# Kernel tuning notes

Measured on AMD Instinct MI355X. Metric: run time of the kernel, lower is better.

## Reference

```python
import jax, jax.numpy as jnp
import numpy as np
import math

D = 1024      # d_model
DC = 256      # d_cache
DL = DC // 4  # d_layer
K = 64        # num_slots
NL = 8        # num_layers
N = NL * K    # cache slots (L*K)
P = 16        # num_patterns
H = 16        # num_heads
B, S = 8, 1024
F = 4 * D

def _linear(x, w, b):
    return jnp.matmul(x, w.T) + b

def _ln(x, g, b):
    m = jnp.mean(x, -1, keepdims=True)
    v = jnp.mean((x - m) ** 2, -1, keepdims=True)
    return (x - m) * jax.lax.rsqrt(v + 1e-5) * g + b

def _mha(q, k, v, wqkv, bqkv, wo, bo, nh):
    # torch nn.MultiheadAttention (batch_first, eval/no-dropout)
    d = q.shape[-1]; dh = d // nh
    wq, wk, wv = jnp.split(wqkv, 3, axis=0)
    bq, bk, bv = jnp.split(bqkv, 3, axis=0)
    qh = _linear(q, wq, bq).reshape(q.shape[0], q.shape[1], nh, dh)
    kh = _linear(k, wk, bk).reshape(k.shape[0], k.shape[1], nh, dh)
    vh = _linear(v, wv, bv).reshape(v.shape[0], v.shape[1], nh, dh)
    s = jnp.einsum('bqhd,bkhd->bhqk', qh, kh) * (1.0 / math.sqrt(dh))
    a = jax.nn.softmax(s, axis=-1)
    o = jnp.einsum('bhqk,bkhd->bqhd', a, vh).reshape(q.shape[0], q.shape[1], d)
    return _linear(o, wo, bo)

def _forward(x, cache, slot_embeddings, layer_ids, gumbel_u, layer_embed,
             attn_wqkv, attn_bqkv, attn_wo, attn_bo,
             pat_wqkv, pat_bqkv, pat_wo, pat_bo, pattern_queries,
             ffn_w1, ffn_b1, ffn_w2, ffn_b2,
             n1_g, n1_b, n2_g, n2_b,
             gate_w, gate_b, sel_w, sel_b, sq_w, sq_b, sk_w, sk_b, an_w, an_b,
             dec_w, dec_b, cq_w, cq_b, ck_w, ck_b, cv_w, cv_b, fg_w, fg_b):
    b, s, d = x.shape
    # --- read_cache: cross-attention from tokens to [B,N,DC] cache slots ---
    cid = jnp.concatenate([cache, jnp.broadcast_to(layer_ids[None], (b,) + layer_ids.shape)], axis=-1)  # [B,N,DC+DL]
    q = _linear(x, cq_w, cq_b)                    # [B,S,DC]
    kk = _linear(cid, ck_w, ck_b)                 # [B,N,DC]
    vv = _linear(cid, cv_w, cv_b)                 # [B,N,DC]
    sc = jnp.einsum('bsd,bnd->bsn', q, kk) * (1.0 / math.sqrt(DC))
    attn = jax.nn.softmax(sc, axis=-1)
    ctx = jnp.einsum('bsn,bnd->bsd', attn, vv)    # [B,S,DC]
    ctx = jnp.concatenate([ctx, jnp.broadcast_to(layer_embed, (b, s, layer_embed.shape[-1]))], axis=-1)
    context = _linear(ctx, dec_w, dec_b)          # [B,S,D]
    # --- gated fusion ---
    gate = jax.nn.sigmoid(_linear(jnp.concatenate([x, context], axis=-1), fg_w, fg_b))
    xf = gate * x + (1.0 - gate) * context
    # --- self-attn + FFN transformer block ---
    xf = _ln(xf + _mha(xf, xf, xf, attn_wqkv, attn_bqkv, attn_wo, attn_bo, H), n1_g, n1_b)
    ffn = _linear(jax.nn.gelu(_linear(xf, ffn_w1, ffn_b1), approximate=False), ffn_w2, ffn_b2)
    y = _ln(xf + ffn, n2_g, n2_b)
    # --- pattern pooling ---
    queries = jnp.broadcast_to(pattern_queries[None], (b,) + pattern_queries.shape)
    patterns = _mha(queries, y, y, pat_wqkv, pat_bqkv, pat_wo, pat_bo, H)   # [B,P,D]
    # --- selection head (hybrid routing + gumbel-softmax, soft mode) ---
    scores = jax.nn.sigmoid(_linear(patterns, gate_w, gate_b))[..., 0]      # [B,P]
    learned = _linear(patterns, sel_w, sel_b)                               # [B,P,K]
    content = jnp.einsum('bpd,kd->bpk', _linear(patterns, sq_w, sq_b),
                         _linear(slot_embeddings, sk_w, sk_b)) * (1.0 / math.sqrt(DC))
    alpha = jax.nn.sigmoid(_linear(patterns, an_w, an_b))                   # [B,P,1]
    logits = alpha * learned + (1.0 - alpha) * content
    g = -jnp.log(-jnp.log(gumbel_u + 1e-8) + 1e-8)
    slot_probs = jax.nn.softmax(logits + g, axis=-1)  # temperature = 1.0, hard=False
    soft_probs = jax.nn.softmax(logits, axis=-1)
    return y, patterns, scores, slot_probs, soft_probs, alpha[..., 0]

def setup_inputs() -> dict:
    key = jax.random.key(0)
    ks = iter(jax.random.split(key, 64))
    def rn(shape, scale=1.0):
        return scale * jax.random.normal(next(ks), shape, dtype=jnp.float32)
    inp = {
        'x': rn((B, S, D)),
        'cache': rn((B, N, DC)),
        'slot_embeddings': rn((K, DC), 0.02),
        'layer_ids': rn((N, DL), 0.02),
        'gumbel_u': jax.random.uniform(next(ks), (B, P, K), dtype=jnp.float32, minval=1e-4, maxval=1.0),
        'layer_embed': rn((1, 1, DL), 0.02),
        'attn_wqkv': rn((3 * D, D), 0.02), 'attn_bqkv': jnp.zeros((3 * D,)),
        'attn_wo': rn((D, D), 0.02), 'attn_bo': jnp.zeros((D,)),
        'pat_wqkv': rn((3 * D, D), 0.02), 'pat_bqkv': jnp.zeros((3 * D,)),
        'pat_wo': rn((D, D), 0.02), 'pat_bo': jnp.zeros((D,)),
        'pattern_queries': rn((P, D), 0.02),
        'ffn_w1': rn((F, D), 0.02), 'ffn_b1': jnp.zeros((F,)),
        'ffn_w2': rn((D, F), 0.02), 'ffn_b2': jnp.zeros((D,)),
        'n1_g': jnp.ones((D,)), 'n1_b': jnp.zeros((D,)),
        'n2_g': jnp.ones((D,)), 'n2_b': jnp.zeros((D,)),
        'gate_w': rn((1, D), 0.02), 'gate_b': jnp.zeros((1,)),
        'sel_w': rn((K, D), 0.02), 'sel_b': jnp.zeros((K,)),
        'sq_w': rn((DC, D), 0.02), 'sq_b': jnp.zeros((DC,)),
        'sk_w': rn((DC, DC), 0.02), 'sk_b': jnp.zeros((DC,)),
        'an_w': rn((1, D), 0.02), 'an_b': jnp.zeros((1,)),
        'dec_w': rn((D, DC + DL), 0.02), 'dec_b': jnp.zeros((D,)),
        'cq_w': rn((DC, D), 0.02), 'cq_b': jnp.zeros((DC,)),
        'ck_w': rn((DC, DC + DL), 0.02), 'ck_b': jnp.zeros((DC,)),
        'cv_w': rn((DC, DC + DL), 0.02), 'cv_b': jnp.zeros((DC,)),
        'fg_w': rn((D, 2 * D), 0.02), 'fg_b': jnp.zeros((D,)),
    }
    return inp

def reference(x, cache, slot_embeddings, layer_ids, gumbel_u, layer_embed,
              attn_wqkv, attn_bqkv, attn_wo, attn_bo,
              pat_wqkv, pat_bqkv, pat_wo, pat_bo, pattern_queries,
              ffn_w1, ffn_b1, ffn_w2, ffn_b2,
              n1_g, n1_b, n2_g, n2_b,
              gate_w, gate_b, sel_w, sel_b, sq_w, sq_b, sk_w, sk_b, an_w, an_b,
              dec_w, dec_b, cq_w, cq_b, ck_w, ck_b, cv_w, cv_b, fg_w, fg_b):
    return _forward(x, cache, slot_embeddings, layer_ids, gumbel_u, layer_embed,
                    attn_wqkv, attn_bqkv, attn_wo, attn_bo,
                    pat_wqkv, pat_bqkv, pat_wo, pat_bo, pattern_queries,
                    ffn_w1, ffn_b1, ffn_w2, ffn_b2,
                    n1_g, n1_b, n2_g, n2_b,
                    gate_w, gate_b, sel_w, sel_b, sq_w, sq_b, sk_w, sk_b, an_w, an_b,
                    dec_w, dec_b, cq_w, cq_b, ck_w, ck_b, cv_w, cv_b, fg_w, fg_b)
```

## Files before the change

kernel.cpp:

```cpp
#include <hip/hip_runtime.h>
#include <math.h>

typedef unsigned short u16;
typedef unsigned int u32;
typedef __bf16 bfx8 __attribute__((ext_vector_type(8)));
typedef float fx4 __attribute__((ext_vector_type(4)));

__device__ __forceinline__ float b2f(u16 v) { return __uint_as_float(((u32)v) << 16); }
__device__ __forceinline__ u16 f2b(float f) {
    u32 u = __float_as_uint(f);
    u32 lsb = (u >> 16) & 1u;
    u += 0x7fffu + lsb;
    return (u16)(u >> 16);
}
__device__ __forceinline__ float4 unpack4(u32 a, u32 b) {
    float4 r;
    r.x = __uint_as_float(a << 16);
    r.y = __uint_as_float(a & 0xffff0000u);
    r.z = __uint_as_float(b << 16);
    r.w = __uint_as_float(b & 0xffff0000u);
    return r;
}
__device__ __forceinline__ float sigmoid_(float x) { return 1.f / (1.f + __expf(-x)); }
__device__ __forceinline__ float gelu_(float x) { return 0.5f * x * (1.f + erff(x * 0.7071067811865475f)); }

__device__ __forceinline__ float ldx(const void* p, long i, int f) {
    return f ? ((const float*)p)[i] : b2f(((const u16*)p)[i]);
}
__device__ __forceinline__ void stx(void* p, long i, float v, int f) {
    if (f) ((float*)p)[i] = v;
    else ((u16*)p)[i] = f2b(v);
}
__device__ __forceinline__ void stage8(u16* dst, const void* src, long idx, int f, bool ok) {
    uint4 r;
    if (!ok) {
        r = make_uint4(0u, 0u, 0u, 0u);
    } else if (f) {
        const float* p = (const float*)src + idx;
        float4 a = *(const float4*)p;
        float4 b = *(const float4*)(p + 4);
        r = make_uint4((u32)f2b(a.x) | ((u32)f2b(a.y) << 16),
                       (u32)f2b(a.z) | ((u32)f2b(a.w) << 16),
                       (u32)f2b(b.x) | ((u32)f2b(b.y) << 16),
                       (u32)f2b(b.z) | ((u32)f2b(b.w) << 16));
    } else {
        r = *(const uint4*)((const u16*)src + idx);
    }
    *(uint4*)dst = r;
}

__device__ __forceinline__ void glds16(const u16* g, u16* l) {
    __builtin_amdgcn_global_load_lds(
        (const __attribute__((address_space(1))) u32*)g,
        (__attribute__((address_space(3))) u32*)l, 16, 0, 0);
}

__global__ void detect_dtype(const u16* __restrict__ n1g, int* __restrict__ flag) {
    *flag = (n1g[0] == 0) ? 1 : 0;
}

__global__ __launch_bounds__(256) void conv_weights(
    const void* awqkv, const void* awo, const void* fw1, const void* fw2,
    const void* pwqkv, const void* fgw, const void* decw, const void* cqw,
    const void* ckw, const void* x, u16* __restrict__ dst, const int* __restrict__ flagp)
{
    const int f = *flagp;
    long c = ((long)blockIdx.x * 256 + threadIdx.x) * 8;
    if (c >= 25837568L) return;
    const void* src; long off;
    if      (c < 3145728L)  { src = awqkv; off = c; }
    else if (c < 4194304L)  { src = awo;   off = c - 3145728L; }
    else if (c < 8388608L)  { src = fw1;   off = c - 4194304L; }
    else if (c < 12582912L) { src = fw2;   off = c - 8388608L; }
    else if (c < 14680064L) { src = pwqkv; off = c - 12582912L + 1048576L; }
    else if (c < 16777216L) { src = fgw;   off = c - 14680064L; }
    else if (c < 17104896L) { src = decw;  off = c - 16777216L; }
    else if (c < 17367040L) { src = cqw;   off = c - 17104896L; }
    else if (c < 17448960L) { src = ckw;   off = c - 17367040L; }
    else                    { src = x;     off = c - 17448960L; }
    uint4 r;
    if (f) {
        const float* p = (const float*)src + off;
        float4 a = *(const float4*)p;
        float4 b = *(const float4*)(p + 4);
        r = make_uint4((u32)f2b(a.x) | ((u32)f2b(a.y) << 16),
                       (u32)f2b(a.z) | ((u32)f2b(a.w) << 16),
                       (u32)f2b(b.x) | ((u32)f2b(b.y) << 16),
                       (u32)f2b(b.z) | ((u32)f2b(b.w) << 16));
    } else {
        r = *(const uint4*)((const u16*)src + off);
    }
    *(uint4*)(dst + c) = r;
}

template <int ACT, int ACC>
__global__ __launch_bounds__(256) void gemm_big(
    const u16* __restrict__ A, const u16* __restrict__ B, const void* __restrict__ bias,
    u16* __restrict__ C, int M, int N, int K, int lda, int ldb, int ldc, float scale,
    long aS, long bS, long cS, long biasBase, const int* __restrict__ flagp)
{
    const int f = *flagp;
    const long z = blockIdx.z;
    const u16* Ab = A + z * aS;
    const u16* Bb = B + z * bS;
    u16* Cb = C + z * cS;

    __shared__ u16 As[8192];
    __shared__ u16 Bs[8192];

    const int tid = threadIdx.x;
    const int w = tid >> 6;
    const int lane = tid & 63;
    const int l15 = lane & 15;
    const int quad = lane >> 4;
    const int wr = w >> 1, wc = w & 1;

    const int m0 = blockIdx.y * 128;
    const int n0 = blockIdx.x * 128;

    const int srow = lane >> 3;
    const int scol = ((lane & 7) ^ srow) << 3;

    fx4 acc[4][4];
#pragma unroll
    for (int mi = 0; mi < 4; ++mi)
#pragma unroll
        for (int ni = 0; ni < 4; ++ni) {
            fx4 zz = {0.f, 0.f, 0.f, 0.f};
            acc[mi][ni] = zz;
        }

    for (int k0 = 0; k0 < K; k0 += 64) {
        __syncthreads();
#pragma unroll
        for (int j = 0; j < 4; ++j) {
            const int rg = (j * 4 + w) * 8 + srow;
            glds16(Ab + (long)(m0 + rg) * lda + k0 + scol, &As[(j * 4 + w) * 512]);
            glds16(Bb + (long)(n0 + rg) * ldb + k0 + scol, &Bs[(j * 4 + w) * 512]);
        }
        __syncthreads();
#pragma unroll
        for (int kk = 0; kk < 2; ++kk) {
            bfx8 af[4], bf[4];
#pragma unroll
            for (int i = 0; i < 4; ++i) {
                const int ar = wr * 64 + i * 16 + l15;
                af[i] = *(const bfx8*)((const char*)As + ar * 128 +
                                       ((kk * 64 + quad * 16) ^ ((ar & 7) << 4)));
                const int br = wc * 64 + i * 16 + l15;
                bf[i] = *(const bfx8*)((const char*)Bs + br * 128 +
                                       ((kk * 64 + quad * 16) ^ ((br & 7) << 4)));
            }
#pragma unroll
            for (int mi = 0; mi < 4; ++mi)
#pragma unroll
                for (int ni = 0; ni < 4; ++ni)
                    acc[mi][ni] = __builtin_amdgcn_mfma_f32_16x16x32_bf16(af[mi], bf[ni], acc[mi][ni], 0, 0, 0);
        }
    }

#pragma unroll
    for (int ni = 0; ni < 4; ++ni) {
        const int col = n0 + wc * 64 + ni * 16 + l15;
        const float bv = bias ? ldx(bias, biasBase + col, f) : 0.f;
#pragma unroll
        for (int mi = 0; mi < 4; ++mi) {
            const int row = m0 + wr * 64 + mi * 16 + quad * 4;
#pragma unroll
            for (int r = 0; r < 4; ++r) {
                float v = acc[mi][ni][r] * scale + bv;
                if (ACT) v = gelu_(v);
                long idx = (long)(row + r) * ldc + col;
                if (ACC) v += b2f(Cb[idx]);
                Cb[idx] = f2b(v);
            }
        }
    }
}

template <int OUTF32, int ACT, int TRANS, int ACC>
__global__ __launch_bounds__(256) void gemm_nt(
    const void* __restrict__ A, const void* __restrict__ B, const void* __restrict__ bias,
    void* __restrict__ Cv, int M, int N, int K, int lda, int ldb, int ldc, float scale,
    long aBase, long aDiv, long aOut, long aIn,
    long bBase, long bDiv, long bOut, long bIn,
    long cDiv, long cOut, long cIn,
    long biasBase, int aIsIn, int bIsIn, int biasIsIn, const int* __restrict__ flagp)
{
    const int dfl = *flagp;
    const int af = aIsIn ? dfl : 0;
    const int bfF = bIsIn ? dfl : 0;
    const int sf = biasIsIn ? dfl : 0;

    long bi = blockIdx.z;
    const long aOff = aBase + (bi / aDiv) * aOut + (bi % aDiv) * aIn;
    const long bOff = bBase + (bi / bDiv) * bOut + (bi % bDiv) * bIn;
    const long cOff = (bi / cDiv) * cOut + (bi % cDiv) * cIn;

    __shared__ u16 As[64][40];
    __shared__ u16 Bs[64][40];

    const int tid = threadIdx.x;
    const int w = tid >> 6;
    const int lane = tid & 63;
    const int m0 = blockIdx.y * 64;
    const int n0 = blockIdx.x * 64;

    const int lr = tid >> 2;
    const int lk = (tid & 3) * 8;

    fx4 acc[4];
#pragma unroll
    for (int c = 0; c < 4; ++c)
#pragma unroll
        for (int r = 0; r < 4; ++r) acc[c][r] = 0.f;

    const int arow = m0 + lr;
    const int brow = n0 + lr;
    const bool aok = arow < M;
    const bool bok = brow < N;

    const int row16 = lane & 15;
    const int quad = lane >> 4;

    for (int k0 = 0; k0 < K; k0 += 32) {
        __syncthreads();
        stage8(&As[lr][lk], A, aOff + (long)arow * lda + k0 + lk, af, aok);
        stage8(&Bs[lr][lk], B, bOff + (long)brow * ldb + k0 + lk, bfF, bok);
        __syncthreads();
        bfx8 afr = *(const bfx8*)&As[w * 16 + row16][quad * 8];
#pragma unroll
        for (int c = 0; c < 4; ++c) {
            bfx8 bfr = *(const bfx8*)&Bs[c * 16 + row16][quad * 8];
            acc[c] = __builtin_amdgcn_mfma_f32_16x16x32_bf16(afr, bfr, acc[c], 0, 0, 0);
        }
    }

#pragma unroll
    for (int c = 0; c < 4; ++c) {
        int col = n0 + c * 16 + row16;
        float bvv = bias ? ldx(bias, biasBase + col, sf) : 0.f;
#pragma unroll
        for (int r = 0; r < 4; ++r) {
            int row = m0 + w * 16 + quad * 4 + r;
            if (row < M) {
                float v = acc[c][r] * scale + bvv;
                if (ACT == 1) v = gelu_(v);
                long idx = TRANS ? ((long)col * ldc + row) : ((long)row * ldc + col);
                if (OUTF32) {
                    ((float*)Cv)[cOff + idx] = v;
                } else {
                    if (ACC) v += b2f(((u16*)Cv)[cOff + idx]);
                    ((u16*)Cv)[cOff + idx] = f2b(v);
                }
            }
        }
    }
}

__global__ __launch_bounds__(256) void attn_self(const u16* __restrict__ QKV, u16* __restrict__ O,
                                                 int ldo, long bStride)
{
    const int h = blockIdx.y;
    const long zoff = (long)blockIdx.z * bStride;
    const u16* Qb = QKV + zoff + h * 64;
    const u16* Kb = Qb + 1024;
    const u16* Vb = Qb + 2048;
    u16* Ob = O + zoff + h * 64;

    const int tid = threadIdx.x;
    const int w = tid >> 6;
    const int lane = tid & 63;
    const int l15 = lane & 15;
    const int quad = lane >> 4;
    const int q0 = blockIdx.x * 64;

    __shared__ u16 Ks[64][72];
    __shared__ u16 Vt[64][72];
    __shared__ u16 Ps[4][16][72];

    bfx8 aq[2];
    {
        const u16* qrow = Qb + (long)(q0 + w * 16 + l15) * 3072 + quad * 8;
        aq[0] = *(const bfx8*)(qrow);
        aq[1] = *(const bfx8*)(qrow + 32);
    }

    fx4 acc[4];
#pragma unroll
    for (int c = 0; c < 4; ++c) {
        fx4 z = {0.f, 0.f, 0.f, 0.f};
        acc[c] = z;
    }
    float m[4], l[4];
#pragma unroll
    for (int r = 0; r < 4; ++r) { m[r] = -__builtin_inff(); l[r] = 0.f; }

    const int sr = tid >> 2;
    const int sc = (tid & 3) * 16;
    const int vr = lane;
    const int vc = w * 16;

    for (int kt = 0; kt < 16; ++kt) {
        __syncthreads();
        {
            const uint4* kp = (const uint4*)(Kb + (long)(kt * 64 + sr) * 3072 + sc);
            *(uint4*)&Ks[sr][sc] = kp[0];
            *(uint4*)&Ks[sr][sc + 8] = kp[1];
        }
        {
            const u16* vp = Vb + (long)(kt * 64 + vr) * 3072 + vc;
            uint4 a = *(const uint4*)vp;
            uint4 b = *(const uint4*)(vp + 8);
            u16 tmp[16];
            *(uint4*)&tmp[0] = a;
            *(uint4*)&tmp[8] = b;
#pragma unroll
            for (int j = 0; j < 16; ++j) Vt[vc + j][vr] = tmp[j];
        }
        __syncthreads();

        fx4 s[4];
#pragma unroll
        for (int c = 0; c < 4; ++c) {
            bfx8 b0 = *(const bfx8*)&Ks[c * 16 + l15][quad * 8];
            bfx8 b1 = *(const bfx8*)&Ks[c * 16 + l15][32 + quad * 8];
            fx4 t = {0.f, 0.f, 0.f, 0.f};
            t = __builtin_amdgcn_mfma_f32_16x16x32_bf16(aq[0], b0, t, 0, 0, 0);
            t = __builtin_amdgcn_mfma_f32_16x16x32_bf16(aq[1], b1, t, 0, 0, 0);
            s[c] = t;
        }
#pragma unroll
        for (int c = 0; c < 4; ++c)
#pragma unroll
            for (int r = 0; r < 4; ++r) s[c][r] *= 0.125f;

#pragma unroll
        for (int r = 0; r < 4; ++r) {
            float tm = fmaxf(fmaxf(s[0][r], s[1][r]), fmaxf(s[2][r], s[3][r]));
#pragma unroll
            for (int off = 1; off < 16; off <<= 1) tm = fmaxf(tm, __shfl_xor(tm, off));
            if (tm > m[r]) {
                float al = __expf(m[r] - tm);
                l[r] *= al;
#pragma unroll
                for (int c = 0; c < 4; ++c) acc[c][r] *= al;
                m[r] = tm;
            }
            float rs = 0.f;
#pragma unroll
            for (int c = 0; c < 4; ++c) {
                float p = __expf(s[c][r] - m[r]);
                s[c][r] = p;
                rs += p;
            }
#pragma unroll
            for (int off = 1; off < 16; off <<= 1) rs += __shfl_xor(rs, off);
            l[r] += rs;
        }

#pragma unroll
        for (int c = 0; c < 4; ++c)
#pragma unroll
            for (int r = 0; r < 4; ++r)
                Ps[w][quad * 4 + r][c * 16 + l15] = f2b(s[c][r]);

#pragma unroll
        for (int ks = 0; ks < 2; ++ks) {
            bfx8 ap = *(const bfx8*)&Ps[w][l15][ks * 32 + quad * 8];
#pragma unroll
            for (int c = 0; c < 4; ++c) {
                bfx8 bv = *(const bfx8*)&Vt[c * 16 + l15][ks * 32 + quad * 8];
                acc[c] = __builtin_amdgcn_mfma_f32_16x16x32_bf16(ap, bv, acc[c], 0, 0, 0);
            }
        }
    }

#pragma unroll
    for (int r = 0; r < 4; ++r) {
        float inv = 1.f / l[r];
        u16* op = Ob + (long)(q0 + w * 16 + quad * 4 + r) * ldo;
#pragma unroll
        for (int c = 0; c < 4; ++c)
            op[c * 16 + l15] = f2b(acc[c][r] * inv);
    }
}

__global__ __launch_bounds__(256) void softmax_inplace(u16* __restrict__ d, int W)
{
    long row = blockIdx.x;
    u16* r = d + row * W;
    int t = threadIdx.x;
    int n = W >> 8;
    float v[4];
    float mx = -1e30f;
    for (int i = 0; i < n; ++i) { v[i] = b2f(r[t + 256 * i]); mx = fmaxf(mx, v[i]); }
    __shared__ float red[256];
    red[t] = mx; __syncthreads();
    for (int s = 128; s > 0; s >>= 1) { if (t < s) red[t] = fmaxf(red[t], red[t + s]); __syncthreads(); }
    mx = red[0]; __syncthreads();
    float sum = 0.f;
    for (int i = 0; i < n; ++i) { v[i] = __expf(v[i] - mx); sum += v[i]; }
    red[t] = sum; __syncthreads();
    for (int s = 128; s > 0; s >>= 1) { if (t < s) red[t] += red[t + s]; __syncthreads(); }
    float inv = 1.f / red[0];
    for (int i = 0; i < n; ++i) r[t + 256 * i] = f2b(v[i] * inv);
}

__global__ __launch_bounds__(256) void add_ln(const u16* __restrict__ a, const u16* __restrict__ rres,
                                              const void* __restrict__ g, const void* __restrict__ be,
                                              u16* __restrict__ o1, void* __restrict__ o2, long o2off,
                                              const int* __restrict__ flagp)
{
    const int f = *flagp;
    long row = blockIdx.x;
    int t = threadIdx.x;
    const u16* ar = a + row * 1024;
    const u16* rr = rres + row * 1024;
    float v[4];
#pragma unroll
    for (int i = 0; i < 4; ++i) { int j = t + 256 * i; v[i] = b2f(ar[j]) + b2f(rr[j]); }
    __shared__ float red[256];
    float s = v[0] + v[1] + v[2] + v[3];
    red[t] = s; __syncthreads();
    for (int k = 128; k > 0; k >>= 1) { if (t < k) red[t] += red[t + k]; __syncthreads(); }
    float mean = red[0] * (1.f / 1024.f);
    __syncthreads();
    float sq = 0.f;
#pragma unroll
    for (int i = 0; i < 4; ++i) { float d = v[i] - mean; sq += d * d; }
    red[t] = sq; __syncthreads();
    for (int k = 128; k > 0; k >>= 1) { if (t < k) red[t] += red[t + k]; __syncthreads(); }
    float rs = rsqrtf(red[0] * (1.f / 1024.f) + 1e-5f);
#pragma unroll
    for (int i = 0; i < 4; ++i) {
        int j = t + 256 * i;
        float y = (v[i] - mean) * rs * ldx(g, j, f) + ldx(be, j, f);
        o1[row * 1024 + j] = f2b(y);
        if (o2) stx(o2, o2off + row * 1024 + j, y, f);
    }
}

__global__ __launch_bounds__(256) void build_cid(const void* __restrict__ cache, const void* __restrict__ lids,
                                                 u16* __restrict__ cid, const int* __restrict__ flagp)
{
    const int f = *flagp;
    long i = (long)blockIdx.x * 256 + threadIdx.x;
    if (i >= 4096L * 320) return;
    long row = i / 320, c = i % 320;
    float v = (c < 256) ? ldx(cache, row * 256 + c, f) : ldx(lids, (row & 511) * 64 + (c - 256), f);
    cid[i] = f2b(v);
}

__global__ __launch_bounds__(256) void fill_ctx_le(const void* __restrict__ le, u16* __restrict__ ctxcat,
                                                   const int* __restrict__ flagp)
{
    const int f = *flagp;
    long i = (long)blockIdx.x * 256 + threadIdx.x;
    if (i >= 8192L * 64) return;
    long row = i >> 6, j = i & 63;
    ctxcat[row * 320 + 256 + j] = f2b(ldx(le, j, f));
}

__global__ __launch_bounds__(256) void fusion(const void* __restrict__ x, const u16* __restrict__ ctx,
                                              u16* __restrict__ gl_xf, const int* __restrict__ flagp)
{
    const int f = *flagp;
    long i = (long)blockIdx.x * 256 + threadIdx.x;
    float gv = sigmoid_(b2f(gl_xf[i]));
    float xv = ldx(x, i, f);
    float cv = b2f(ctx[i]);
    gl_xf[i] = f2b(gv * xv + (1.f - gv) * cv);
}

__global__ __launch_bounds__(256) void cast_pat(const float* __restrict__ pf, u16* __restrict__ pb,
                                                void* __restrict__ pout, long poff,
                                                const int* __restrict__ flagp)
{
    const int f = *flagp;
    long i = (long)blockIdx.x * 256 + threadIdx.x;
    if (i >= 131072L) return;
    float v = pf[i];
    pb[i] = f2b(v);
    stx(pout, poff + i, v, f);
}

__global__ __launch_bounds__(64) void pat_pv(const u16* __restrict__ patp, const u16* __restrict__ kv,
                                             u16* __restrict__ opat, long pStride, long kvStride, long oStride)
{
    int qi = blockIdx.x, h = blockIdx.y, z = blockIdx.z, t = threadIdx.x;
    const u16* prow = patp + (long)z * pStride + ((long)(h * 16 + qi)) * 1024;
    const u16* v = kv + (long)z * kvStride + 1024 + h * 64 + t;
    float o = 0.f;
#pragma unroll 4
    for (int key = 0; key < 1024; ++key) o += b2f(prow[key]) * b2f(v[(long)key * 2048]);
    opat[(long)z * oStride + (long)qi * 1024 + h * 64 + t] = f2b(o);
}

__global__ __launch_bounds__(64) void final_head(const u16* __restrict__ patb, const float* __restrict__ learned,
                                                 const float* __restrict__ content, const void* __restrict__ gum,
                                                 const void* __restrict__ gw, const void* __restrict__ gb,
                                                 const void* __restrict__ anw, const void* __restrict__ anb,
                                                 void* __restrict__ outp, long oSC, long oSLOT, long oSOFT, long oAL,
                                                 const int* __restrict__ flagp)
{
    const int f = *flagp;
    int row = blockIdx.x;
    int t = threadIdx.x;
    float pa = 0.f, ps = 0.f;
    for (int j = t; j < 1024; j += 64) {
        float p = b2f(patb[(long)row * 1024 + j]);
        pa += p * ldx(anw, j, f);
        ps += p * ldx(gw, j, f);
    }
#pragma unroll
    for (int off = 32; off > 0; off >>= 1) { pa += __shfl_xor(pa, off); ps += __shfl_xor(ps, off); }
    float alpha = sigmoid_(pa + ldx(anb, 0, f));
    float score = sigmoid_(ps + ldx(gb, 0, f));
    float logit = alpha * learned[row * 64 + t] + (1.f - alpha) * content[row * 64 + t];
    float u = ldx(gum, row * 64 + t, f);
    float inner = -logf(u + 1e-8f) + 1e-8f;
    inner = fmaxf(inner, 1e-20f);
    float gg = -logf(inner);
    float l1 = logit + gg, l2 = logit;
    float m1 = l1, m2 = l2;
#pragma unroll
    for (int off = 32; off > 0; off >>= 1) { m1 = fmaxf(m1, __shfl_xor(m1, off)); m2 = fmaxf(m2, __shfl_xor(m2, off)); }
    float e1 = __expf(l1 - m1), e2 = __expf(l2 - m2);
    float s1 = e1, s2 = e2;
#pragma unroll
    for (int off = 32; off > 0; off >>= 1) { s1 += __shfl_xor(s1, off); s2 += __shfl_xor(s2, off); }
    stx(outp, oSLOT + row * 64 + t, e1 / s1, f);
    stx(outp, oSOFT + row * 64 + t, e2 / s2, f);
    if (t == 0) { stx(outp, oSC + row, score, f); stx(outp, oAL + row, alpha, f); }
}

static void launch_gemm(hipStream_t st, int outf32, int act, int trans, int acc,
                        const void* A, const void* B, const void* bias, void* C,
                        int M, int N, int K, int lda, int ldb, int ldc, float scale, int batch,
                        long aBase, long aD, long aO, long aI,
                        long bBase, long bD, long bO, long bI,
                        long cD, long cO, long cI,
                        long biasBase, int aIsIn, int bIsIn, int biasIsIn, const int* flagp)
{
    dim3 g(N / 64, (M + 63) / 64, batch);
#define PASS A, B, bias, C, M, N, K, lda, ldb, ldc, scale, aBase, aD, aO, aI, bBase, bD, bO, bI, \
             cD, cO, cI, biasBase, aIsIn, bIsIn, biasIsIn, flagp
    if (outf32)      gemm_nt<1, 0, 0, 0><<<g, 256, 0, st>>>(PASS);
    else if (act)    gemm_nt<0, 1, 0, 0><<<g, 256, 0, st>>>(PASS);
    else if (trans)  gemm_nt<0, 0, 1, 0><<<g, 256, 0, st>>>(PASS);
    else if (acc)    gemm_nt<0, 0, 0, 1><<<g, 256, 0, st>>>(PASS);
    else             gemm_nt<0, 0, 0, 0><<<g, 256, 0, st>>>(PASS);
#undef PASS
}

static void launch_big(hipStream_t st, int act, int acc,
                       const u16* A, const u16* B, const void* bias, u16* C,
                       int M, int N, int K, int lda, int ldb, int ldc, float scale, int batch,
                       long aS, long bS, long cS, long biasBase, const int* flagp)
{
    dim3 g(N / 128, M / 128, batch);
#define PASSB A, B, bias, C, M, N, K, lda, ldb, ldc, scale, aS, bS, cS, biasBase, flagp
    if (act)      gemm_big<1, 0><<<g, 256, 0, st>>>(PASSB);
    else if (acc) gemm_big<0, 1><<<g, 256, 0, st>>>(PASSB);
    else          gemm_big<0, 0><<<g, 256, 0, st>>>(PASSB);
#undef PASSB
}

#define WS_CID     0L
#define WS_QB      2621440L
#define WS_KKB     6815744L
#define WS_VVT     8912896L
#define WS_SC      11010048L
#define WS_CTXCAT  0L
#define WS_CONTEXT 16777216L
#define WS_XF      0L

#define CS_QKVB    33554432L
#define CS_PROJ    16777216L
#define CS_FFN1C   16777216L
#define CS_FFN2C   33554432L
#define CS_KVPATB  16777216L
#define CS_QPAT    20971520L
#define CS_PATSC   21004288L
#define CS_OPAT    21528576L
#define CS_PATF32  21790720L
#define CS_PATB    22315008L
#define CS_LEARN   22577152L
#define CS_SQP     22609920L
#define CS_SKE     22675456L
#define CS_CONT    22708224L
#define CS_FLAG    39845888L
#define CS_NEED    39845892L

#define FP_QKV     33554432L
#define FP_PROJ    16777216L
#define FP_FFN1    33554432L
#define FP_FFN2    16777216L
#define FP_KVPAT   33554432L
#define FP_PATSC   16777216L
#define FP_QPAT    100663296L
#define FP_OPAT    100696064L
#define FP_PATF32  100958208L
#define FP_PATB    101482496L
#define FP_LEARN   101744640L
#define FP_SQP     101777408L
#define FP_SKE     101842944L
#define FP_CONT    101875712L
#define FP_FLAG    101908480L
#define FP_NEED    101908484L

#define FP2_WB     102760448L
#define WB_AWQKV   0L
#define WB_AWO     3145728L
#define WB_FW1     4194304L
#define WB_FW2     8388608L
#define WB_PWKV    12582912L
#define WB_FGW     14680064L
#define WB_DECW    16777216L
#define WB_CQW     17104896L
#define WB_CKW     17367040L
#define WB_X       17448960L
#define WB_TOTAL   25837568L
#define FP2_NEED   (FP2_WB + WB_TOTAL * 2)

#define OUT_Y      0L
#define OUT_PAT    8388608L
#define OUT_SCORES 8519680L
#define OUT_SLOT   8519808L
#define OUT_SOFT   8528000L
#define OUT_ALPHA  8536192L

extern "C" void kernel_launch(void* const* d_in, const int* in_sizes, int n_in,
                              void* d_out, int out_size, void* d_ws, size_t ws_size,
                              hipStream_t stream)
{
    const void* x     = d_in[0];
    const void* cache = d_in[1];
    const void* slote = d_in[2];
    const void* lids  = d_in[3];
    const void* gum   = d_in[4];
    const void* le    = d_in[5];
    const void* awqkv = d_in[6];
    const void* abqkv = d_in[7];
    const void* awo   = d_in[8];
    const void* abo   = d_in[9];
    const void* pwqkv = d_in[10];
    const void* pbqkv = d_in[11];
    const void* pwo   = d_in[12];
    const void* pbo   = d_in[13];
    const void* pq    = d_in[14];
    const void* fw1   = d_in[15];
    const void* fb1   = d_in[16];
    const void* fw2   = d_in[17];
    const void* fb2   = d_in[18];
    const void* n1g   = d_in[19];
    const void* n1b   = d_in[20];
    const void* n2g   = d_in[21];
    const void* n2b   = d_in[22];
    const void* gw    = d_in[23];
    const void* gb    = d_in[24];
    const void* selw  = d_in[25];
    const void* selb  = d_in[26];
    const void* sqw   = d_in[27];
    const void* sqb   = d_in[28];
    const void* skw   = d_in[29];
    const void* skb   = d_in[30];
    const void* anw   = d_in[31];
    const void* anb   = d_in[32];
    const void* decw  = d_in[33];
    const void* decb  = d_in[34];
    const void* cqw   = d_in[35];
    const void* cqb   = d_in[36];
    const void* ckw   = d_in[37];
    const void* ckb   = d_in[38];
    const void* cvw   = d_in[39];
    const void* cvb   = d_in[40];
    const void* fgw   = d_in[41];
    const void* fgb   = d_in[42];

    char* ws = (char*)d_ws;
    auto W  = [&](long off) { return (u16*)(ws + off); };
    auto Wf = [&](long off) { return (float*)(ws + off); };

    const bool fast = ws_size >= (size_t)FP_NEED;
    const bool fast2 = ws_size >= (size_t)FP2_NEED;
    int* flg = (int*)(ws + (fast ? FP_FLAG : CS_FLAG));
    u16* WB = (u16*)(ws + FP2_WB);
    const long oQPAT   = fast ? FP_QPAT   : CS_QPAT;
    const long oOPAT   = fast ? FP_OPAT   : CS_OPAT;
    const long oPATF32 = fast ? FP_PATF32 : CS_PATF32;
    const long oPATB   = fast ? FP_PATB   : CS_PATB;
    const long oLEARN  = fast ? FP_LEARN  : CS_LEARN;
    const long oSQP    = fast ? FP_SQP    : CS_SQP;
    const long oSKE    = fast ? FP_SKE    : CS_SKE;
    const long oCONT   = fast ? FP_CONT   : CS_CONT;

    detect_dtype<<<1, 1, 0, stream>>>((const u16*)n1g, flg);
    if (fast2)
        conv_weights<<<12616, 256, 0, stream>>>(awqkv, awo, fw1, fw2, pwqkv, fgw, decw, cqw, ckw, x, WB, flg);
    build_cid<<<dim3((4096 * 320 + 255) / 256), 256, 0, stream>>>(cache, lids, W(WS_CID), flg);
    if (fast2)
        launch_big(stream, 0, 0, WB + WB_X, WB + WB_CQW, cqb, W(WS_QB), 8192, 256, 1024,
                   1024, 1024, 256, 1.f, 1, 0, 0, 0, 0, flg);
    else
        launch_gemm(stream, 0, 0, 0, 0, x, cqw, cqb, W(WS_QB), 8192, 256, 1024, 1024, 1024, 256, 1.f, 1,
                    0, 1, 0, 0, 0, 1, 0, 0, 1, 0, 0, 0, 1, 1, 1, flg);
    if (fast2)
        launch_big(stream, 0, 0, W(WS_CID), WB + WB_CKW, ckb, W(WS_KKB), 4096, 256, 320,
                   320, 320, 256, 1.f, 1, 0, 0, 0, 0, flg);
    else
        launch_gemm(stream, 0, 0, 0, 0, W(WS_CID), ckw, ckb, W(WS_KKB), 4096, 256, 320, 320, 320, 256, 1.f, 1,
                    0, 1, 0, 0, 0, 1, 0, 0, 1, 0, 0, 0, 0, 1, 1, flg);
    launch_gemm(stream, 0, 0, 1, 0, W(WS_CID), cvw, cvb, W(WS_VVT), 512, 256, 320, 320, 320, 512, 1.f, 8,
                0, 1, 163840, 0, 0, 1, 0, 0, 1, 131072, 0, 0, 0, 1, 1, flg);
    if (fast2)
        launch_big(stream, 0, 0, W(WS_QB), W(WS_KKB), nullptr, W(WS_SC), 1024, 512, 256,
                   256, 256, 512, 0.0625f, 8, 262144, 131072, 524288, 0, flg);
    else
        launch_gemm(stream, 0, 0, 0, 0, W(WS_QB), W(WS_KKB), nullptr, W(WS_SC), 1024, 512, 256, 256, 256, 512,
                    0.0625f, 8, 0, 1, 262144, 0, 0, 1, 131072, 0, 1, 524288, 0, 0, 0, 0, 0, flg);
    softmax_inplace<<<8192, 256, 0, stream>>>(W(WS_SC), 512);
    if (fast2)
        launch_big(stream, 0, 0, W(WS_SC), W(WS_VVT), nullptr, W(WS_CTXCAT), 1024, 256, 512,
                   512, 512, 320, 1.f, 8, 524288, 131072, 327680, 0, flg);
    else
        launch_gemm(stream, 0, 0, 0, 0, W(WS_SC), W(WS_VVT), nullptr, W(WS_CTXCAT), 1024, 256, 512, 512, 512, 320,
                    1.f, 8, 0, 1, 524288, 0, 0, 1, 131072, 0, 1, 327680, 0, 0, 0, 0, 0, flg);
    fill_ctx_le<<<dim3((8192 * 64 + 255) / 256), 256, 0, stream>>>(le, W(WS_CTXCAT), flg);
    if (fast2)
        launch_big(stream, 0, 0, W(WS_CTXCAT), WB + WB_DECW, decb, W(WS_CONTEXT), 8192, 1024, 320,
                   320, 320, 1024, 1.f, 1, 0, 0, 0, 0, flg);
    else
        launch_gemm(stream, 0, 0, 0, 0, W(WS_CTXCAT), decw, decb, W(WS_CONTEXT), 8192, 1024, 320, 320, 320, 1024,
                    1.f, 1, 0, 1, 0, 0, 0, 1, 0, 0, 1, 0, 0, 0, 0, 1, 1, flg);
    if (fast2)
        launch_big(stream, 0, 0, WB + WB_X, WB + WB_FGW, fgb, W(WS_XF), 8192, 1024, 1024,
                   1024, 2048, 1024, 1.f, 1, 0, 0, 0, 0, flg);
    else
        launch_gemm(stream, 0, 0, 0, 0, x, fgw, fgb, W(WS_XF), 8192, 1024, 1024, 1024, 2048, 1024, 1.f, 1,
                    0, 1, 0, 0, 0, 1, 0, 0, 1, 0, 0, 0, 1, 1, 1, flg);
    if (fast2)
        launch_big(stream, 0, 1, W(WS_CONTEXT), WB + WB_FGW + 1024, nullptr, W(WS_XF), 8192, 1024, 1024,
                   1024, 2048, 1024, 1.f, 1, 0, 0, 0, 0, flg);
    else
        launch_gemm(stream, 0, 0, 0, 1, W(WS_CONTEXT), fgw, nullptr, W(WS_XF), 8192, 1024, 1024, 1024, 2048, 1024,
                    1.f, 1, 0, 1, 0, 0, 1024, 1, 0, 0, 1, 0, 0, 0, 0, 1, 0, flg);
    fusion<<<32768, 256, 0, stream>>>(x, W(WS_CONTEXT), W(WS_XF), flg);

    if (fast) {
        if (fast2)
            launch_big(stream, 0, 0, W(WS_XF), WB + WB_AWQKV, abqkv, W(FP_QKV), 8192, 3072, 1024,
                       1024, 1024, 3072, 1.f, 1, 0, 0, 0, 0, flg);
        else
            launch_gemm(stream, 0, 0, 0, 0, W(WS_XF), awqkv, abqkv, W(FP_QKV), 8192, 3072, 1024,
                        1024, 1024, 3072, 1.f, 1, 0, 1, 0, 0, 0, 1, 0, 0, 1, 0, 0, 0, 0, 1, 1, flg);
        attn_self<<<dim3(16, 16, 8), 256, 0, stream>>>(W(FP_QKV), W(FP_QKV), 3072, 3145728L);
        if (fast2)
            launch_big(stream, 0, 0, W(FP_QKV), WB + WB_AWO, abo, W(FP_PROJ), 8192, 1024, 1024,
                       3072, 1024, 1024, 1.f, 1, 0, 0, 0, 0, flg);
        else
            launch_gemm(stream, 0, 0, 0, 0, W(FP_QKV), awo, abo, W(FP_PROJ), 8192, 1024, 1024,
                        3072, 1024, 1024, 1.f, 1, 0, 1, 0, 0, 0, 1, 0, 0, 1, 0, 0, 0, 0, 1, 1, flg);
        add_ln<<<8192, 256, 0, stream>>>(W(WS_XF), W(FP_PROJ), n1g, n1b, W(WS_XF), nullptr, 0, flg);
        if (fast2)
            launch_big(stream, 1, 0, W(WS_XF), WB + WB_FW1, fb1, W(FP_FFN1), 8192, 4096, 1024,
                       1024, 1024, 4096, 1.f, 1, 0, 0, 0, 0, flg);
        else
            launch_gemm(stream, 0, 1, 0, 0, W(WS_XF), fw1, fb1, W(FP_FFN1), 8192, 4096, 1024,
                        1024, 1024, 4096, 1.f, 1, 0, 1, 0, 0, 0, 1, 0, 0, 1, 0, 0, 0, 0, 1, 1, flg);
        if (fast2)
            launch_big(stream, 0, 0, W(FP_FFN1), WB + WB_FW2, fb2, W(FP_FFN2), 8192, 1024, 4096,
                       4096, 4096, 1024, 1.f, 1, 0, 0, 0, 0, flg);
        else
            launch_gemm(stream, 0, 0, 0, 0, W(FP_FFN1), fw2, fb2, W(FP_FFN2), 8192, 1024, 4096,
                        4096, 4096, 1024, 1.f, 1, 0, 1, 0, 0, 0, 1, 0, 0, 1, 0, 0, 0, 0, 1, 1, flg);
        add_ln<<<8192, 256, 0, stream>>>(W(WS_XF), W(FP_FFN2), n2g, n2b, W(WS_XF), d_out, OUT_Y, flg);
        launch_gemm(stream, 0, 0, 0, 0, pq, pwqkv, pbqkv, W(oQPAT), 16, 1024, 1024, 1024, 1024, 1024, 1.f, 1,
                    0, 1, 0, 0, 0, 1, 0, 0, 1, 0, 0, 0, 1, 1, 1, flg);
        if (fast2)
            launch_big(stream, 0, 0, W(WS_XF), WB + WB_PWKV, pbqkv, W(FP_KVPAT), 8192, 2048, 1024,
                       1024, 1024, 2048, 1.f, 1, 0, 0, 0, 1024, flg);
        else
            launch_gemm(stream, 0, 0, 0, 0, W(WS_XF), pwqkv, pbqkv, W(FP_KVPAT), 8192, 2048, 1024,
                        1024, 1024, 2048, 1.f, 1, 0, 1, 0, 0, 1048576, 1, 0, 0, 1, 0, 0, 1024, 0, 1, 1, flg);
        launch_gemm(stream, 0, 0, 0, 0, W(oQPAT), W(FP_KVPAT), nullptr, W(FP_PATSC), 16, 1024, 64,
                    1024, 2048, 1024, 0.125f, 128,
                    0, 16, 0, 64, 0, 16, 2097152, 64, 1, 16384, 0, 0, 0, 0, 0, flg);
        softmax_inplace<<<2048, 256, 0, stream>>>(W(FP_PATSC), 1024);
        pat_pv<<<dim3(16, 16, 8), 64, 0, stream>>>(W(FP_PATSC), W(FP_KVPAT), W(oOPAT),
                                                   262144L, 2097152L, 16384L);
    } else {
        for (int b = 0; b < 8; ++b) {
            launch_gemm(stream, 0, 0, 0, 0, W(WS_XF) + (long)b * 1048576, awqkv, abqkv, W(CS_QKVB),
                        1024, 3072, 1024, 1024, 1024, 3072, 1.f, 1,
                        0, 1, 0, 0, 0, 1, 0, 0, 1, 0, 0, 0, 0, 1, 1, flg);
            attn_self<<<dim3(16, 16, 1), 256, 0, stream>>>(W(CS_QKVB), W(CS_QKVB), 3072, 0L);
            launch_gemm(stream, 0, 0, 0, 0, W(CS_QKVB), awo, abo, W(CS_PROJ) + (long)b * 1048576,
                        1024, 1024, 1024, 3072, 1024, 1024, 1.f, 1,
                        0, 1, 0, 0, 0, 1, 0, 0, 1, 0, 0, 0, 0, 1, 1, flg);
        }
        add_ln<<<8192, 256, 0, stream>>>(W(WS_XF), W(CS_PROJ), n1g, n1b, W(WS_XF), nullptr, 0, flg);
        for (int c = 0; c < 4; ++c) {
            u16* xf2c = W(WS_XF) + (long)c * 2048 * 1024;
            launch_gemm(stream, 0, 1, 0, 0, xf2c, fw1, fb1, W(CS_FFN1C), 2048, 4096, 1024, 1024, 1024, 4096,
                        1.f, 1, 0, 1, 0, 0, 0, 1, 0, 0, 1, 0, 0, 0, 0, 1, 1, flg);
            launch_gemm(stream, 0, 0, 0, 0, W(CS_FFN1C), fw2, fb2, W(CS_FFN2C), 2048, 1024, 4096,
                        4096, 4096, 1024, 1.f, 1, 0, 1, 0, 0, 0, 1, 0, 0, 1, 0, 0, 0, 0, 1, 1, flg);
            add_ln<<<2048, 256, 0, stream>>>(xf2c, W(CS_FFN2C), n2g, n2b, xf2c, d_out,
                                             OUT_Y + (long)c * 2048 * 1024, flg);
        }
        launch_gemm(stream, 0, 0, 0, 0, pq, pwqkv, pbqkv, W(oQPAT), 16, 1024, 1024, 1024, 1024, 1024, 1.f, 1,
                    0, 1, 0, 0, 0, 1, 0, 0, 1, 0, 0, 0, 1, 1, 1, flg);
        for (int b = 0; b < 8; ++b) {
            const u16* yb = W(WS_XF) + (long)b * 1048576;
            launch_gemm(stream, 0, 0, 0, 0, yb, pwqkv, pbqkv, W(CS_KVPATB), 1024, 2048, 1024,
                        1024, 1024, 2048, 1.f, 1, 0, 1, 0, 0, 1048576, 1, 0, 0, 1, 0, 0, 1024, 0, 1, 1, flg);
            launch_gemm(stream, 0, 0, 0, 0, W(oQPAT), W(CS_KVPATB), nullptr, W(CS_PATSC), 16, 1024, 64,
                        1024, 2048, 1024, 0.125f, 16,
                        0, 16, 0, 64, 0, 16, 0, 64, 1, 16384, 0, 0, 0, 0, 0, flg);
            softmax_inplace<<<256, 256, 0, stream>>>(W(CS_PATSC), 1024);
            pat_pv<<<dim3(16, 16, 1), 64, 0, stream>>>(W(CS_PATSC), W(CS_KVPATB),
                                                       W(oOPAT) + (long)b * 16384, 0L, 0L, 0L);
        }
    }

    launch_gemm(stream, 1, 0, 0, 0, W(oOPAT), pwo, pbo, Wf(oPATF32), 128, 1024, 1024, 1024, 1024, 1024,
                1.f, 1, 0, 1, 0, 0, 0, 1, 0, 0, 1, 0, 0, 0, 0, 1, 1, flg);
    cast_pat<<<512, 256, 0, stream>>>(Wf(oPATF32), W(oPATB), d_out, OUT_PAT, flg);
    launch_gemm(stream, 1, 0, 0, 0, W(oPATB), selw, selb, Wf(oLEARN), 128, 64, 1024, 1024, 1024, 64,
                1.f, 1, 0, 1, 0, 0, 0, 1, 0, 0, 1, 0, 0, 0, 0, 1, 1, flg);
    launch_gemm(stream, 0, 0, 0, 0, W(oPATB), sqw, sqb, W(oSQP), 128, 256, 1024, 1024, 1024, 256, 1.f, 1,
                0, 1, 0, 0, 0, 1, 0, 0, 1, 0, 0, 0, 0, 1, 1, flg);
    launch_gemm(stream, 0, 0, 0, 0, slote, skw, skb, W(oSKE), 64, 256, 256, 256, 256, 256, 1.f, 1,
                0, 1, 0, 0, 0, 1, 0, 0, 1, 0, 0, 0, 1, 1, 1, flg);
    launch_gemm(stream, 1, 0, 0, 0, W(oSQP), W(oSKE), nullptr, Wf(oCONT), 128, 64, 256, 256, 256, 64,
                0.0625f, 1, 0, 1, 0, 0, 0, 1, 0, 0, 1, 0, 0, 0, 0, 0, 0, flg);
    final_head<<<128, 64, 0, stream>>>(W(oPATB), Wf(oLEARN), Wf(oCONT), gum, gw, gb, anw, anb,
                                       d_out, OUT_SCORES, OUT_SLOT, OUT_SOFT, OUT_ALPHA, flg);
}
```

Before: 1.174 ms.

## Add flash-style attention with pre-transposed V, XCD-aware GEMM tiling, vectorized elementwise

Replaces the self-attention kernel with an online-softmax MFMA kernel. A new pre-pass writes V transposed per head so it can be loaded into LDS with async global-to-LDS copies. The big GEMM remaps block indices so that consecutive tiles land on the same XCD for better L2 locality. add_ln and the gating fusion kernel are vectorized to 8-byte and 16-byte accesses, with the fusion launch grid shrunk to match. The cost is an extra transpose kernel and a scratch buffer aliased at FP_VT, which shares its offset with FP_PROJ and is only safe because the projection is written after attention finishes.

```diff
diff --git a/kernel.cpp b/kernel.cpp
--- a/kernel.cpp
+++ b/kernel.cpp
@@ -115,8 +115,14 @@
     const int quad = lane >> 4;
     const int wr = w >> 1, wc = w & 1;
 
-    const int m0 = blockIdx.y * 128;
-    const int n0 = blockIdx.x * 128;
+    const int gx = gridDim.x;
+    const int nwg = gx * gridDim.y;
+    const int o = blockIdx.y * gx + blockIdx.x;
+    const int q_ = nwg >> 3, r_ = nwg & 7;
+    const int xcd = o & 7, idx = o >> 3;
+    const int wg = (xcd < r_ ? xcd * (q_ + 1) : r_ * (q_ + 1) + (xcd - r_) * q_) + idx;
+    const int m0 = (wg / gx) * 128;
+    const int n0 = (wg % gx) * 128;
 
     const int srow = lane >> 3;
     const int scol = ((lane & 7) ^ srow) << 3;
@@ -170,9 +176,9 @@
             for (int r = 0; r < 4; ++r) {
                 float v = acc[mi][ni][r] * scale + bv;
                 if (ACT) v = gelu_(v);
-                long idx = (long)(row + r) * ldc + col;
-                if (ACC) v += b2f(Cb[idx]);
-                Cb[idx] = f2b(v);
+                long idx2 = (long)(row + r) * ldc + col;
+                if (ACC) v += b2f(Cb[idx2]);
+                Cb[idx2] = f2b(v);
             }
         }
     }
@@ -255,6 +261,166 @@
                 }
             }
         }
+    }
+}
+
+__global__ __launch_bounds__(256) void vt_prep(const u16* __restrict__ QKV, u16* __restrict__ VtG)
+{
+    const int kc = blockIdx.x;
+    const int h  = blockIdx.y;
+    const int b  = blockIdx.z;
+    const int t  = threadIdx.x;
+    __shared__ u16 Ls[64][72];
+    const u16* src = QKV + (long)b * 3145728L + 2048 + h * 64;
+    {
+        int kr = t >> 2;
+        int c0 = t & 3;
+#pragma unroll
+        for (int half = 0; half < 2; ++half) {
+            int lc = c0 + half * 4;
+            int pc = lc ^ (kr & 7);
+            uint4 v = *(const uint4*)(src + (long)(kc * 64 + kr) * 3072 + lc * 8);
+            *(uint4*)&Ls[kr][pc * 8] = v;
+        }
+    }
+    __syncthreads();
+    {
+        int d = t >> 2;
+        int k0 = (t & 3) * 16;
+        u16 tmp[16];
+#pragma unroll
+        for (int j = 0; j < 16; ++j) {
+            int key = k0 + j;
+            int pc = (d >> 3) ^ (key & 7);
+            tmp[j] = Ls[key][pc * 8 + (d & 7)];
+        }
+        u16* dst = VtG + ((long)(b * 16 + h) * 64 + d) * 1024 + kc * 64 + k0;
+        *(uint4*)(dst) = *(uint4*)&tmp[0];
+        *(uint4*)(dst + 8) = *(uint4*)&tmp[8];
+    }
+}
+
+__global__ __launch_bounds__(256) void attn_fast(const u16* __restrict__ QKV, u16* __restrict__ O,
+                                                 const u16* __restrict__ VtG, int ldo, long bStride)
+{
+    const int h = blockIdx.y;
+    const long zoff = (long)blockIdx.z * bStride;
+    const u16* Qb = QKV + zoff + h * 64;
+    const u16* Kb = Qb + 1024;
+    u16* Ob = O + zoff + h * 64;
+    const u16* Vg = VtG + (long)(blockIdx.z * 16 + h) * 65536L;
+
+    const int tid = threadIdx.x;
+    const int w = tid >> 6;
+    const int lane = tid & 63;
+    const int l15 = lane & 15;
+    const int quad = lane >> 4;
+    const int q0 = blockIdx.x * 64;
+
+    __shared__ u16 Ks[4096];
+    __shared__ u16 Vs[4096];
+    __shared__ u16 Ps[4][16][72];
+
+    bfx8 aq[2];
+    {
+        const u16* qrow = Qb + (long)(q0 + w * 16 + l15) * 3072 + quad * 8;
+        aq[0] = *(const bfx8*)(qrow);
+        aq[1] = *(const bfx8*)(qrow + 32);
+    }
+
+    fx4 acc[4];
+#pragma unroll
+    for (int c = 0; c < 4; ++c) {
+        fx4 z = {0.f, 0.f, 0.f, 0.f};
+        acc[c] = z;
+    }
+    float m[4], l[4];
+#pragma unroll
+    for (int r = 0; r < 4; ++r) { m[r] = -__builtin_inff(); l[r] = 0.f; }
+
+    const int srow = lane >> 3;
+    const int scol = ((lane & 7) ^ srow) << 3;
+
+    for (int kt = 0; kt < 16; ++kt) {
+        __syncthreads();
+        {
+            const int g0 = w, g1 = w + 4;
+            glds16(Kb + (long)(kt * 64 + g0 * 8 + srow) * 3072 + scol, &Ks[g0 * 512]);
+            glds16(Kb + (long)(kt * 64 + g1 * 8 + srow) * 3072 + scol, &Ks[g1 * 512]);
+            glds16(Vg + (long)(g0 * 8 + srow) * 1024 + kt * 64 + scol, &Vs[g0 * 512]);
+            glds16(Vg + (long)(g1 * 8 + srow) * 1024 + kt * 64 + scol, &Vs[g1 * 512]);
+        }
+        __syncthreads();
+
+        fx4 s[4];
+#pragma unroll
+        for (int c = 0; c < 4; ++c) {
+            const int kr = c * 16 + l15;
+            const char* kb_ = (const char*)Ks + kr * 128;
+            const int sw = (kr & 7) << 4;
+            bfx8 b0 = *(const bfx8*)(kb_ + ((quad * 16) ^ sw));
+            bfx8 b1 = *(const bfx8*)(kb_ + ((64 + quad * 16) ^ sw));
+            fx4 t = {0.f, 0.f, 0.f, 0.f};
+            t = __builtin_amdgcn_mfma_f32_16x16x32_bf16(aq[0], b0, t, 0, 0, 0);
+            t = __builtin_amdgcn_mfma_f32_16x16x32_bf16(aq[1], b1, t, 0, 0, 0);
+            s[c] = t;
+        }
+#pragma unroll
+        for (int c = 0; c < 4; ++c)
+#pragma unroll
+            for (int r = 0; r < 4; ++r) s[c][r] *= 0.125f;
+
+#pragma unroll
+        for (int r = 0; r < 4; ++r) {
+            float tm = fmaxf(fmaxf(s[0][r], s[1][r]), fmaxf(s[2][r], s[3][r]));
+#pragma unroll
+            for (int off = 1; off < 16; off <<= 1) tm = fmaxf(tm, __shfl_xor(tm, off));
+            if (tm > m[r]) {
+                float al = __expf(m[r] - tm);
+                l[r] *= al;
+#pragma unroll
+                for (int c = 0; c < 4; ++c) acc[c][r] *= al;
+                m[r] = tm;
+            }
+            float rs = 0.f;
+#pragma unroll
+            for (int c = 0; c < 4; ++c) {
+                float p = __expf(s[c][r] - m[r]);
+                s[c][r] = p;
+                rs += p;
+            }
+#pragma unroll
+            for (int off = 1; off < 16; off <<= 1) rs += __shfl_xor(rs, off);
+            l[r] += rs;
+        }
+
+#pragma unroll
+        for (int c = 0; c < 4; ++c)
+#pragma unroll
+            for (int r = 0; r < 4; ++r)
+                Ps[w][quad * 4 + r][c * 16 + l15] = f2b(s[c][r]);
+
+#pragma unroll
+        for (int ks = 0; ks < 2; ++ks) {
+            bfx8 ap = *(const bfx8*)&Ps[w][l15][ks * 32 + quad * 8];
+#pragma unroll
+            for (int c = 0; c < 4; ++c) {
+                const int vr = c * 16 + l15;
+                const int sw = (vr & 7) << 4;
+                bfx8 bv = *(const bfx8*)((const char*)Vs + vr * 128 +
+                                         ((ks * 64 + quad * 16) ^ sw));
+                acc[c] = __builtin_amdgcn_mfma_f32_16x16x32_bf16(ap, bv, acc[c], 0, 0, 0);
+            }
+        }
+    }
+
+#pragma unroll
+    for (int r = 0; r < 4; ++r) {
+        float inv = 1.f / l[r];
+        u16* op = Ob + (long)(q0 + w * 16 + quad * 4 + r) * ldo;
+#pragma unroll
+        for (int c = 0; c < 4; ++c)
+            op[c * 16 + l15] = f2b(acc[c][r] * inv);
     }
 }
 
@@ -415,11 +581,15 @@
     const int f = *flagp;
     long row = blockIdx.x;
     int t = threadIdx.x;
-    const u16* ar = a + row * 1024;
-    const u16* rr = rres + row * 1024;
+    const int j0 = t * 4;
+    const u16* ar = a + row * 1024 + j0;
+    const u16* rr = rres + row * 1024 + j0;
+    u16 av[4], rv[4];
+    *(uint2*)av = *(const uint2*)ar;
+    *(uint2*)rv = *(const uint2*)rr;
     float v[4];
 #pragma unroll
-    for (int i = 0; i < 4; ++i) { int j = t + 256 * i; v[i] = b2f(ar[j]) + b2f(rr[j]); }
+    for (int i = 0; i < 4; ++i) v[i] = b2f(av[i]) + b2f(rv[i]);
     __shared__ float red[256];
     float s = v[0] + v[1] + v[2] + v[3];
     red[t] = s; __syncthreads();
@@ -432,12 +602,21 @@
     red[t] = sq; __syncthreads();
     for (int k = 128; k > 0; k >>= 1) { if (t < k) red[t] += red[t + k]; __syncthreads(); }
     float rs = rsqrtf(red[0] * (1.f / 1024.f) + 1e-5f);
-#pragma unroll
-    for (int i = 0; i < 4; ++i) {
-        int j = t + 256 * i;
-        float y = (v[i] - mean) * rs * ldx(g, j, f) + ldx(be, j, f);
-        o1[row * 1024 + j] = f2b(y);
-        if (o2) stx(o2, o2off + row * 1024 + j, y, f);
+    float y[4];
+#pragma unroll
+    for (int i = 0; i < 4; ++i)
+        y[i] = (v[i] - mean) * rs * ldx(g, j0 + i, f) + ldx(be, j0 + i, f);
+    u16 ob[4];
+#pragma unroll
+    for (int i = 0; i < 4; ++i) ob[i] = f2b(y[i]);
+    *(uint2*)(o1 + row * 1024 + j0) = *(const uint2*)ob;
+    if (o2) {
+        if (f) {
+            float4 o4; o4.x = y[0]; o4.y = y[1]; o4.z = y[2]; o4.w = y[3];
+            *(float4*)((float*)o2 + o2off + row * 1024 + j0) = o4;
+        } else {
+            *(uint2*)((u16*)o2 + o2off + row * 1024 + j0) = *(const uint2*)ob;
+        }
     }
 }
 
@@ -466,11 +645,29 @@
                                               u16* __restrict__ gl_xf, const int* __restrict__ flagp)
 {
     const int f = *flagp;
-    long i = (long)blockIdx.x * 256 + threadIdx.x;
-    float gv = sigmoid_(b2f(gl_xf[i]));
-    float xv = ldx(x, i, f);
-    float cv = b2f(ctx[i]);
-    gl_xf[i] = f2b(gv * xv + (1.f - gv) * cv);
+    long i = ((long)blockIdx.x * 256 + threadIdx.x) * 8;
+    u16 gl[8], cv[8];
+    *(uint4*)gl = *(const uint4*)(gl_xf + i);
+    *(uint4*)cv = *(const uint4*)(ctx + i);
+    float xv[8];
+    if (f) {
+        const float* xp = (const float*)x + i;
+        float4 a = *(const float4*)xp, b = *(const float4*)(xp + 4);
+        xv[0] = a.x; xv[1] = a.y; xv[2] = a.z; xv[3] = a.w;
+        xv[4] = b.x; xv[5] = b.y; xv[6] = b.z; xv[7] = b.w;
+    } else {
+        u16 xb[8];
+        *(uint4*)xb = *(const uint4*)((const u16*)x + i);
+#pragma unroll
+        for (int j = 0; j < 8; ++j) xv[j] = b2f(xb[j]);
+    }
+    u16 out[8];
+#pragma unroll
+    for (int j = 0; j < 8; ++j) {
+        float gv = sigmoid_(b2f(gl[j]));
+        out[j] = f2b(gv * xv[j] + (1.f - gv) * b2f(cv[j]));
+    }
+    *(uint4*)(gl_xf + i) = *(const uint4*)out;
 }
 
 __global__ __launch_bounds__(256) void cast_pat(const float* __restrict__ pf, u16* __restrict__ pb,
@@ -594,6 +791,7 @@
 #define CS_NEED    39845892L
 
 #define FP_QKV     33554432L
+#define FP_VT      16777216L
 #define FP_PROJ    16777216L
 #define FP_FFN1    33554432L
 #define FP_FFN2    16777216L
@@ -746,7 +944,7 @@
     else
         launch_gemm(stream, 0, 0, 0, 1, W(WS_CONTEXT), fgw, nullptr, W(WS_XF), 8192, 1024, 1024, 1024, 2048, 1024,
                     1.f, 1, 0, 1, 0, 0, 1024, 1, 0, 0, 1, 0, 0, 0, 0, 1, 0, flg);
-    fusion<<<32768, 256, 0, stream>>>(x, W(WS_CONTEXT), W(WS_XF), flg);
+    fusion<<<4096, 256, 0, stream>>>(x, W(WS_CONTEXT), W(WS_XF), flg);
 
     if (fast) {
         if (fast2)
@@ -755,7 +953,8 @@
         else
             launch_gemm(stream, 0, 0, 0, 0, W(WS_XF), awqkv, abqkv, W(FP_QKV), 8192, 3072, 1024,
                         1024, 1024, 3072, 1.f, 1, 0, 1, 0, 0, 0, 1, 0, 0, 1, 0, 0, 0, 0, 1, 1, flg);
-        attn_self<<<dim3(16, 16, 8), 256, 0, stream>>>(W(FP_QKV), W(FP_QKV), 3072, 3145728L);
+        vt_prep<<<dim3(16, 16, 8), 256, 0, stream>>>(W(FP_QKV), W(FP_VT));
+        attn_fast<<<dim3(16, 16, 8), 256, 0, stream>>>(W(FP_QKV), W(FP_QKV), W(FP_VT), 3072, 3145728L);
         if (fast2)
             launch_big(stream, 0, 0, W(FP_QKV), WB + WB_AWO, abo, W(FP_PROJ), 8192, 1024, 1024,
                        3072, 1024, 1024, 1.f, 1, 0, 0, 0, 0, flg);
```

Result: slower. 1.219 ms (+3.9%).
